# Kernel optimization log

Measured on AMD Instinct MI355X. Metric: run time of the kernel, lower is better.

The kernel has to match this reference:

```python
import jax, jax.numpy as jnp
import numpy as np

N = 50000      # nodes
E = 300000     # edges
F_IN = 128     # num_features
H = 256        # hidden_dim
C = 32         # num_classes


def gcn_conv(x, src, dst, W, b, num_nodes):
    """PyG-style GCNConv: add self-loops, sym-normalize, X W, scatter-add, + bias."""
    loop = jnp.arange(num_nodes, dtype=src.dtype)
    src2 = jnp.concatenate([src, loop])          # [E+N]
    dst2 = jnp.concatenate([dst, loop])          # [E+N]
    # degree of target nodes (with self-loops, unit edge weights)
    deg = jax.ops.segment_sum(jnp.ones_like(dst2, dtype=x.dtype), dst2,
                              num_segments=num_nodes)
    dinv = jnp.where(deg > 0, jax.lax.rsqrt(deg), 0.0)
    norm = dinv[src2] * dinv[dst2]               # [E+N]
    h = x @ W                                    # [N, out]  dense GEMM first (PyG order)
    msg = h[src2] * norm[:, None]                # gather + scale  [E+N, out]
    out = jax.ops.segment_sum(msg, dst2, num_segments=num_nodes)  # scatter-add
    return out + b


def setup_inputs() -> dict:
    key = jax.random.key(0)
    ks = jax.random.split(key, 8)
    x = jax.random.normal(ks[0], (N, F_IN), dtype=jnp.float32)
    edge_index = jax.random.randint(ks[1], (2, E), 0, N, dtype=jnp.int64)
    W1 = jax.random.normal(ks[2], (F_IN, H), dtype=jnp.float32) / np.float32(np.sqrt(F_IN))
    b1 = jnp.zeros((H,), jnp.float32)
    W2 = jax.random.normal(ks[3], (H, H), dtype=jnp.float32) / np.float32(np.sqrt(H))
    b2 = jnp.zeros((H,), jnp.float32)
    Wc = jax.random.normal(ks[4], (H, C), dtype=jnp.float32) / np.float32(np.sqrt(H))
    bc = jnp.zeros((C,), jnp.float32)
    return {"x": x, "edge_index": edge_index, "W1": W1, "b1": b1,
            "W2": W2, "b2": b2, "Wc": Wc, "bc": bc}


def reference(x, edge_index, W1, b1, W2, b2, Wc, bc):
    src, dst = edge_index[0], edge_index[1]
    h = gcn_conv(x, src, dst, W1, b1, N)
    h = jax.nn.relu(h)                 # dropout is identity in eval mode
    h = gcn_conv(h, src, dst, W2, b2, N)
    h = jax.nn.relu(h)
    return h @ Wc + bc                 # [N, C]
```

## Files before the change

### kernel.cpp

```cpp
#include <hip/hip_runtime.h>
#include <math.h>

using short8 = __attribute__((ext_vector_type(8))) short;
using f32x4 = __attribute__((ext_vector_type(4))) float;

#define CAP 48

__device__ inline short f2bf(float f) {
    unsigned u = __builtin_bit_cast(unsigned, f);
    unsigned r = (u + 0x7fffu + ((u >> 16) & 1u)) >> 16;
    return (short)r;
}
__device__ inline float bf2f(short s) {
    unsigned u = ((unsigned)(unsigned short)s) << 16;
    return __builtin_bit_cast(float, u);
}

typedef const void __attribute__((address_space(1))) gvoid_t;
typedef void __attribute__((address_space(3))) svoid_t;
__device__ inline void gload16(const short* g, short* l) {
    __builtin_amdgcn_global_load_lds((gvoid_t*)g, (svoid_t*)l, 16, 0, 0);
}


__global__ void prep_kernel(const float* __restrict__ x, const float* __restrict__ W1,
                            const float* __restrict__ W2, const float* __restrict__ Wc,
                            const int* __restrict__ src, const int* __restrict__ dst,
                            short* __restrict__ xb, short* __restrict__ Wt1,
                            short* __restrict__ Wt2, short* __restrict__ Wtc,
                            int* __restrict__ deg, int* __restrict__ eslot,
                            int n, int e) {
    int idx = blockIdx.x * blockDim.x + threadIdx.x;
    const int nx8 = n * 16;
    if (idx < nx8) {
        const float4* p = (const float4*)x + (size_t)idx * 2;
        float4 v0 = p[0], v1 = p[1];
        short8 o;
        o[0] = f2bf(v0.x); o[1] = f2bf(v0.y); o[2] = f2bf(v0.z); o[3] = f2bf(v0.w);
        o[4] = f2bf(v1.x); o[5] = f2bf(v1.y); o[6] = f2bf(v1.z); o[7] = f2bf(v1.w);
        ((short8*)xb)[idx] = o;
        return;
    }
    idx -= nx8;
    if (idx < 128 * 256) {
        int k = idx >> 8, c = idx & 255;
        Wt1[c * 128 + k] = f2bf(W1[idx]);
        return;
    }
    idx -= 128 * 256;
    if (idx < 256 * 256) {
        int k = idx >> 8, c = idx & 255;
        Wt2[c * 256 + k] = f2bf(W2[idx]);
        return;
    }
    idx -= 256 * 256;
    if (idx < 256 * 32) {
        int k = idx >> 5, c = idx & 31;
        Wtc[c * 256 + k] = f2bf(Wc[idx]);
        return;
    }
    idx -= 256 * 32;
    if (idx < e) {
        int d = dst[idx], s = src[idx];
        int pos = atomicAdd(&deg[d], 1);
        if (pos < CAP) eslot[(size_t)d * CAP + pos] = s;
    }
}


template<bool RELU_BF16OUT>
__global__ __launch_bounds__(256) void mfma_gemm128_kernel(
    const short* __restrict__ A, const short* __restrict__ Wt,
    const float* __restrict__ bias, void* __restrict__ Cout,
    int M, int K, int NC)
{
    __shared__ short As[128 * 32];
    __shared__ short Bs[128 * 32];

    const int tid = threadIdx.x;
    const int wave = tid >> 6, lane = tid & 63;
    const int m0 = blockIdx.y * 128, n0 = blockIdx.x * 128;
    const int wm = (wave >> 1) * 64, wn = (wave & 1) * 64;

    const int lr0 = tid >> 2;
    const int lr1 = 64 + lr0;
    const int cdst = tid & 3;
    const int cg0 = cdst ^ ((lr0 >> 1) & 3);
    const int cg1 = cdst ^ ((lr1 >> 1) & 3);
    int ga0 = m0 + lr0; if (ga0 >= M) ga0 = M - 1;
    int ga1 = m0 + lr1; if (ga1 >= M) ga1 = M - 1;
    int gb0 = n0 + lr0; if (gb0 >= NC) gb0 = NC - 1;
    int gb1 = n0 + lr1; if (gb1 >= NC) gb1 = NC - 1;
    const short* pa0 = A + (size_t)ga0 * K + cg0 * 8;
    const short* pa1 = A + (size_t)ga1 * K + cg1 * 8;
    const short* pb0 = Wt + (size_t)gb0 * K + cg0 * 8;
    const short* pb1 = Wt + (size_t)gb1 * K + cg1 * 8;

    short* lA0 = &As[(wave * 16) * 32];
    short* lA1 = &As[(64 + wave * 16) * 32];
    short* lB0 = &Bs[(wave * 16) * 32];
    short* lB1 = &Bs[(64 + wave * 16) * 32];

    f32x4 acc[4][4] = {};
    const int fr = lane & 15;
    const int cfrag = lane >> 4;
    const int swzr = (fr >> 1) & 3;

    for (int k0 = 0; k0 < K; k0 += 32) {
        gload16(pa0 + k0, lA0);
        gload16(pa1 + k0, lA1);
        gload16(pb0 + k0, lB0);
        gload16(pb1 + k0, lB1);
        __syncthreads();

        short8 af[4], bfv[4];
        #pragma unroll
        for (int mt = 0; mt < 4; ++mt) {
            int rr = wm + mt * 16 + fr;
            af[mt] = *(const short8*)&As[rr * 32 + ((cfrag ^ swzr) << 3)];
        }
        #pragma unroll
        for (int nt = 0; nt < 4; ++nt) {
            int rr = wn + nt * 16 + fr;
            bfv[nt] = *(const short8*)&Bs[rr * 32 + ((cfrag ^ swzr) << 3)];
        }

        #pragma unroll
        for (int mt = 0; mt < 4; ++mt)
            #pragma unroll
            for (int nt = 0; nt < 4; ++nt)
                acc[mt][nt] = __builtin_amdgcn_mfma_f32_16x16x32_bf16(
                    af[mt], bfv[nt], acc[mt][nt], 0, 0, 0);

        __syncthreads();
    }

    #pragma unroll
    for (int mt = 0; mt < 4; ++mt) {
        #pragma unroll
        for (int nt = 0; nt < 4; ++nt) {
            #pragma unroll
            for (int r = 0; r < 4; ++r) {
                int grow = m0 + wm + mt * 16 + (lane >> 4) * 4 + r;
                int gcol = n0 + wn + nt * 16 + (lane & 15);
                if (grow < M && gcol < NC) {
                    float v = acc[mt][nt][r] + bias[gcol];
                    if (RELU_BF16OUT)
                        ((short*)Cout)[(size_t)grow * NC + gcol] = f2bf(fmaxf(v, 0.f));
                    else
                        ((float*)Cout)[(size_t)grow * NC + gcol] = v;
                }
            }
        }
    }
}


__global__ __launch_bounds__(512, 4) void layer2_fused_kernel(
    const short* __restrict__ hA,
    const int* __restrict__ deg, const int* __restrict__ eslot,
    const short* __restrict__ Wt2,
    const float* __restrict__ b2,
    const short* __restrict__ Wtc,
    const float* __restrict__ bc,
    float* __restrict__ out,
    int M)
{
    const int K = 256;
    __shared__ short smem[128 * 256 + 256 * 32];
    short* hT = smem;
    short* Bs = smem + 128 * 256;

    const int tid = threadIdx.x;
    const int wave = tid >> 6, lane = tid & 63;
    const int m0 = blockIdx.x * 128;

    const int srow = tid >> 2;
    const int cdst = tid & 3;
    const int lrB0 = srow, lrB1 = 128 + srow;
    const int cg0 = cdst ^ ((lrB0 >> 1) & 3);
    const int cg1 = cdst ^ ((lrB1 >> 1) & 3);
    const short* pb0 = Wt2 + (size_t)lrB0 * K + cg0 * 8;
    const short* pb1 = Wt2 + (size_t)lrB1 * K + cg1 * 8;
    short* lB0 = &Bs[(wave * 16) * 32];
    short* lB1 = &Bs[(128 + wave * 16) * 32];

    gload16(pb0, lB0);
    gload16(pb1, lB1);

    {
        const int grp = tid >> 5;
        const int gl  = tid & 31;
        const int f   = gl * 8;
        const int wslot = (gl >> 2) * 32;
        for (int r0 = 0; r0 < 128; r0 += 16) {
            int r = r0 + grp;
            int node = m0 + r; if (node >= M) node = M - 1;
            int dg = deg[node];
            if (dg > CAP) dg = CAP;
            float di = rsqrtf((float)dg + 1.0f);
            float w = di * di;
            short8 hv = *(const short8*)(hA + (size_t)node * 256 + f);
            float a[8];
            #pragma unroll
            for (int j = 0; j < 8; ++j) a[j] = bf2f(hv[j]) * w;

            const int* bucket = eslot + (size_t)node * CAP;
            for (int e = 0; e < dg; e += 4) {
                int4 s4 = *(const int4*)(bucket + e);
                int i0 = s4.x;
                int i1 = (e + 1 < dg) ? s4.y : 0;
                int i2 = (e + 2 < dg) ? s4.z : 0;
                int i3 = (e + 3 < dg) ? s4.w : 0;
                int d0 = deg[i0], d1 = deg[i1], d2 = deg[i2], d3 = deg[i3];
                short8 v0 = *(const short8*)(hA + (size_t)i0 * 256 + f);
                short8 v1 = *(const short8*)(hA + (size_t)i1 * 256 + f);
                short8 v2 = *(const short8*)(hA + (size_t)i2 * 256 + f);
                short8 v3 = *(const short8*)(hA + (size_t)i3 * 256 + f);
                float w0 = rsqrtf((float)d0 + 1.0f) * di;
                float w1 = (e + 1 < dg) ? rsqrtf((float)d1 + 1.0f) * di : 0.f;
                float w2 = (e + 2 < dg) ? rsqrtf((float)d2 + 1.0f) * di : 0.f;
                float w3 = (e + 3 < dg) ? rsqrtf((float)d3 + 1.0f) * di : 0.f;
                #pragma unroll
                for (int j = 0; j < 8; ++j) {
                    a[j] = fmaf(bf2f(v0[j]), w0, a[j]);
                    a[j] = fmaf(bf2f(v1[j]), w1, a[j]);
                    a[j] = fmaf(bf2f(v2[j]), w2, a[j]);
                    a[j] = fmaf(bf2f(v3[j]), w3, a[j]);
                }
            }
            short8 o;
            #pragma unroll
            for (int j = 0; j < 8; ++j) o[j] = f2bf(a[j]);
            int slot = (gl & 3) ^ ((r >> 1) & 3);
            *(short8*)&hT[r * 256 + wslot + slot * 8] = o;
        }
    }

    const int wm = (wave >> 2) * 64;
    const int wn = (wave & 3) * 64;
    const int fr = lane & 15;
    const int cfrag = lane >> 4;
    const int swzr = (fr >> 1) & 3;

    f32x4 acc[4][4] = {};
    for (int k0 = 0; k0 < K; k0 += 32) {
        __syncthreads();

        short8 af[4], bfv[4];
        #pragma unroll
        for (int mt = 0; mt < 4; ++mt) {
            int rr = wm + mt * 16 + fr;
            af[mt] = *(const short8*)&hT[rr * 256 + k0 + ((cfrag ^ swzr) << 3)];
        }
        #pragma unroll
        for (int nt = 0; nt < 4; ++nt) {
            int rr = wn + nt * 16 + fr;
            bfv[nt] = *(const short8*)&Bs[rr * 32 + ((cfrag ^ swzr) << 3)];
        }

        __syncthreads();
        if (k0 + 32 < K) {
            gload16(pb0 + k0 + 32, lB0);
            gload16(pb1 + k0 + 32, lB1);
        }

        #pragma unroll
        for (int mt = 0; mt < 4; ++mt)
            #pragma unroll
            for (int nt = 0; nt < 4; ++nt)
                acc[mt][nt] = __builtin_amdgcn_mfma_f32_16x16x32_bf16(
                    af[mt], bfv[nt], acc[mt][nt], 0, 0, 0);
    }

    #pragma unroll
    for (int mt = 0; mt < 4; ++mt) {
        #pragma unroll
        for (int nt = 0; nt < 4; ++nt) {
            #pragma unroll
            for (int r = 0; r < 4; ++r) {
                int lrow = wm + mt * 16 + (lane >> 4) * 4 + r;
                int gcol = wn + nt * 16 + fr;
                float v = acc[mt][nt][r] + b2[gcol];
                int slot = ((gcol >> 3) & 3) ^ ((lrow >> 1) & 3);
                hT[lrow * 256 + (gcol >> 5) * 32 + slot * 8 + (gcol & 7)] =
                    f2bf(fmaxf(v, 0.f));
            }
        }
    }
    __syncthreads();

    f32x4 c2[2] = {};
    for (int k0 = 0; k0 < K; k0 += 32) {
        int row = wave * 16 + fr;
        short8 a8 = *(const short8*)&hT[row * 256 + k0 + ((cfrag ^ swzr) << 3)];
        #pragma unroll
        for (int nt = 0; nt < 2; ++nt) {
            short8 b8 = *(const short8*)(Wtc + (size_t)(nt * 16 + fr) * K +
                                         (cfrag << 3) + k0);
            c2[nt] = __builtin_amdgcn_mfma_f32_16x16x32_bf16(a8, b8, c2[nt], 0, 0, 0);
        }
    }
    #pragma unroll
    for (int nt = 0; nt < 2; ++nt) {
        #pragma unroll
        for (int r = 0; r < 4; ++r) {
            int grow = m0 + wave * 16 + (lane >> 4) * 4 + r;
            int gcol = nt * 16 + fr;
            if (grow < M)
                out[(size_t)grow * 32 + gcol] = c2[nt][r] + bc[gcol];
        }
    }
}


template<int LPN>
__global__ __launch_bounds__(256) void gather_kernel(
    const short* __restrict__ h, const int* __restrict__ deg,
    const int* __restrict__ eslot, short* __restrict__ out, int n)
{
    const int F = LPN * 8;
    int node = (blockIdx.x * 256 + threadIdx.x) / LPN;
    if (node >= n) return;
    int lane = threadIdx.x % LPN;
    int f = lane * 8;

    int dg = deg[node];
    if (dg > CAP) dg = CAP;
    float di = rsqrtf((float)dg + 1.0f);
    float w = di * di;

    const size_t rb = (size_t)node * F + f;
    short8 hv = *(const short8*)(h + rb);
    float a[8];
    #pragma unroll
    for (int j = 0; j < 8; ++j) a[j] = bf2f(hv[j]) * w;

    const int* bucket = eslot + (size_t)node * CAP;
    for (int e = 0; e < dg; e += 4) {
        int4 s4 = *(const int4*)(bucket + e);
        int i0 = s4.x;
        int i1 = (e + 1 < dg) ? s4.y : 0;
        int i2 = (e + 2 < dg) ? s4.z : 0;
        int i3 = (e + 3 < dg) ? s4.w : 0;
        int d0 = deg[i0], d1 = deg[i1], d2 = deg[i2], d3 = deg[i3];
        short8 v0 = *(const short8*)(h + (size_t)i0 * F + f);
        short8 v1 = *(const short8*)(h + (size_t)i1 * F + f);
        short8 v2 = *(const short8*)(h + (size_t)i2 * F + f);
        short8 v3 = *(const short8*)(h + (size_t)i3 * F + f);
        float w0 = rsqrtf((float)d0 + 1.0f) * di;
        float w1 = (e + 1 < dg) ? rsqrtf((float)d1 + 1.0f) * di : 0.f;
        float w2 = (e + 2 < dg) ? rsqrtf((float)d2 + 1.0f) * di : 0.f;
        float w3 = (e + 3 < dg) ? rsqrtf((float)d3 + 1.0f) * di : 0.f;
        #pragma unroll
        for (int j = 0; j < 8; ++j) {
            a[j] = fmaf(bf2f(v0[j]), w0, a[j]);
            a[j] = fmaf(bf2f(v1[j]), w1, a[j]);
            a[j] = fmaf(bf2f(v2[j]), w2, a[j]);
            a[j] = fmaf(bf2f(v3[j]), w3, a[j]);
        }
    }
    short8 o;
    #pragma unroll
    for (int j = 0; j < 8; ++j) o[j] = f2bf(a[j]);
    *(short8*)(out + rb) = o;
}


extern "C" void kernel_launch(void* const* d_in, const int* in_sizes, int n_in,
                              void* d_out, int out_size, void* d_ws, size_t ws_size,
                              hipStream_t stream) {
    const float* x  = (const float*)d_in[0];
    const int*   ei = (const int*)d_in[1];
    const float* W1 = (const float*)d_in[2];
    const float* b1 = (const float*)d_in[3];
    const float* W2 = (const float*)d_in[4];
    const float* b2 = (const float*)d_in[5];
    const float* Wc = (const float*)d_in[6];
    const float* bc = (const float*)d_in[7];
    float* out = (float*)d_out;

    const int E = in_sizes[1] / 2;
    const int N = in_sizes[0] / 128;
    const int F_IN = 128, H = 256;
    const int* src = ei;
    const int* dst = ei + E;

    short* xb   = (short*)d_ws;
    short* aggX = xb + (size_t)N * 128;
    short* hA   = aggX + (size_t)N * 128;
    short* Wt1  = hA + (size_t)N * 256;
    short* Wt2  = Wt1 + 256 * 128;
    short* Wtc  = Wt2 + 256 * 256;
    int*   deg  = (int*)(Wtc + 32 * 256);
    int*   eslot= deg + N;

    const int TB = 256;

    hipMemsetAsync(deg, 0, (size_t)N * sizeof(int), stream);

    const int prep_total = N * 16 + 128 * 256 + 256 * 256 + 256 * 32 + E;
    prep_kernel<<<(prep_total + TB - 1) / TB, TB, 0, stream>>>(
        x, W1, W2, Wc, src, dst, xb, Wt1, Wt2, Wtc, deg, eslot, N, E);

    const int gy = (N + 127) / 128;

    gather_kernel<16><<<((size_t)N * 16 + TB - 1) / TB, TB, 0, stream>>>(
        xb, deg, eslot, aggX, N);
    mfma_gemm128_kernel<true><<<dim3(H / 128, gy), 256, 0, stream>>>(aggX, Wt1, b1, hA, N, F_IN, H);

    layer2_fused_kernel<<<gy, 512, 0, stream>>>(
        hA, deg, eslot, Wt2, b2, Wtc, bc, out, N);
}
```

Measured before the change: 195.1 us.

## Read W2 fragments straight from global and pad the LDS tile instead of swizzling

The fused layer-2 kernel no longer stages W2 tiles into LDS with async global-to-LDS loads and per-k-step barriers. B fragments are now read directly from global memory (cache-resident W2), and the aggregated tile uses a padded row stride (264) instead of an XOR swizzle. This removes two barriers per k-step and frees LDS. In exchange, global load latency sits in the MFMA loop, and the 16-byte padding may leave some LDS bank conflicts.

```diff
diff --git a/kernel.cpp b/kernel.cpp
--- a/kernel.cpp
+++ b/kernel.cpp
@@ -167,32 +167,17 @@
     int M)
 {
     const int K = 256;
-    __shared__ short smem[128 * 256 + 256 * 32];
-    short* hT = smem;
-    short* Bs = smem + 128 * 256;
+    const int TP = 264;
+    __shared__ short hT[128 * 264];
 
     const int tid = threadIdx.x;
     const int wave = tid >> 6, lane = tid & 63;
     const int m0 = blockIdx.x * 128;
-
-    const int srow = tid >> 2;
-    const int cdst = tid & 3;
-    const int lrB0 = srow, lrB1 = 128 + srow;
-    const int cg0 = cdst ^ ((lrB0 >> 1) & 3);
-    const int cg1 = cdst ^ ((lrB1 >> 1) & 3);
-    const short* pb0 = Wt2 + (size_t)lrB0 * K + cg0 * 8;
-    const short* pb1 = Wt2 + (size_t)lrB1 * K + cg1 * 8;
-    short* lB0 = &Bs[(wave * 16) * 32];
-    short* lB1 = &Bs[(128 + wave * 16) * 32];
-
-    gload16(pb0, lB0);
-    gload16(pb1, lB1);
 
     {
         const int grp = tid >> 5;
         const int gl  = tid & 31;
         const int f   = gl * 8;
-        const int wslot = (gl >> 2) * 32;
         for (int r0 = 0; r0 < 128; r0 += 16) {
             int r = r0 + grp;
             int node = m0 + r; if (node >= M) node = M - 1;
@@ -232,38 +217,25 @@
             short8 o;
             #pragma unroll
             for (int j = 0; j < 8; ++j) o[j] = f2bf(a[j]);
-            int slot = (gl & 3) ^ ((r >> 1) & 3);
-            *(short8*)&hT[r * 256 + wslot + slot * 8] = o;
-        }
-    }
+            *(short8*)&hT[r * TP + f] = o;
+        }
+    }
+    __syncthreads();
 
     const int wm = (wave >> 2) * 64;
     const int wn = (wave & 3) * 64;
     const int fr = lane & 15;
-    const int cfrag = lane >> 4;
-    const int swzr = (fr >> 1) & 3;
+    const int fk = (lane >> 4) * 8;
 
     f32x4 acc[4][4] = {};
     for (int k0 = 0; k0 < K; k0 += 32) {
-        __syncthreads();
-
         short8 af[4], bfv[4];
         #pragma unroll
-        for (int mt = 0; mt < 4; ++mt) {
-            int rr = wm + mt * 16 + fr;
-            af[mt] = *(const short8*)&hT[rr * 256 + k0 + ((cfrag ^ swzr) << 3)];
-        }
-        #pragma unroll
-        for (int nt = 0; nt < 4; ++nt) {
-            int rr = wn + nt * 16 + fr;
-            bfv[nt] = *(const short8*)&Bs[rr * 32 + ((cfrag ^ swzr) << 3)];
-        }
-
-        __syncthreads();
-        if (k0 + 32 < K) {
-            gload16(pb0 + k0 + 32, lB0);
-            gload16(pb1 + k0 + 32, lB1);
-        }
+        for (int mt = 0; mt < 4; ++mt)
+            af[mt] = *(const short8*)&hT[(wm + mt * 16 + fr) * TP + k0 + fk];
+        #pragma unroll
+        for (int nt = 0; nt < 4; ++nt)
+            bfv[nt] = *(const short8*)(Wt2 + (size_t)(wn + nt * 16 + fr) * K + k0 + fk);
 
         #pragma unroll
         for (int mt = 0; mt < 4; ++mt)
@@ -272,6 +244,7 @@
                 acc[mt][nt] = __builtin_amdgcn_mfma_f32_16x16x32_bf16(
                     af[mt], bfv[nt], acc[mt][nt], 0, 0, 0);
     }
+    __syncthreads();
 
     #pragma unroll
     for (int mt = 0; mt < 4; ++mt) {
@@ -282,9 +255,7 @@
                 int lrow = wm + mt * 16 + (lane >> 4) * 4 + r;
                 int gcol = wn + nt * 16 + fr;
                 float v = acc[mt][nt][r] + b2[gcol];
-                int slot = ((gcol >> 3) & 3) ^ ((lrow >> 1) & 3);
-                hT[lrow * 256 + (gcol >> 5) * 32 + slot * 8 + (gcol & 7)] =
-                    f2bf(fmaxf(v, 0.f));
+                hT[lrow * TP + gcol] = f2bf(fmaxf(v, 0.f));
             }
         }
     }
@@ -292,12 +263,10 @@
 
     f32x4 c2[2] = {};
     for (int k0 = 0; k0 < K; k0 += 32) {
-        int row = wave * 16 + fr;
-        short8 a8 = *(const short8*)&hT[row * 256 + k0 + ((cfrag ^ swzr) << 3)];
+        short8 a8 = *(const short8*)&hT[(wave * 16 + fr) * TP + k0 + fk];
         #pragma unroll
         for (int nt = 0; nt < 2; ++nt) {
-            short8 b8 = *(const short8*)(Wtc + (size_t)(nt * 16 + fr) * K +
-                                         (cfrag << 3) + k0);
+            short8 b8 = *(const short8*)(Wtc + (size_t)(nt * 16 + fr) * K + k0 + fk);
             c2[nt] = __builtin_amdgcn_mfma_f32_16x16x32_bf16(a8, b8, c2[nt], 0, 0, 0);
         }
     }
```

New measurement: 200.5 us. 2.8% more time.

## Fuse layer-1 neighbor aggregation into the layer-1 MFMA GEMM kernel

Applied to the files above, without the earlier changes.

Replaces the separate gather kernel and the layer-1 GEMM with one kernel. Each 512-thread block aggregates 128 node rows of normalized neighbor features into an LDS tile (XOR-swizzled), then multiplies that tile by W1 with bf16 MFMA while prefetching the next W1 slab. This removes the aggX round trip through global memory and one launch. In exchange, each block computes all 256 output columns, uses more LDS, and runs the irregular gather at lower parallelism than the standalone gather kernel.

```diff
diff --git a/kernel.cpp b/kernel.cpp
--- a/kernel.cpp
+++ b/kernel.cpp
@@ -68,71 +68,116 @@
 }
 
 
-template<bool RELU_BF16OUT>
-__global__ __launch_bounds__(256) void mfma_gemm128_kernel(
-    const short* __restrict__ A, const short* __restrict__ Wt,
-    const float* __restrict__ bias, void* __restrict__ Cout,
-    int M, int K, int NC)
+__global__ __launch_bounds__(512, 4) void layer1_fused_kernel(
+    const short* __restrict__ xb,
+    const int* __restrict__ deg, const int* __restrict__ eslot,
+    const short* __restrict__ Wt1,
+    const float* __restrict__ b1,
+    short* __restrict__ hA,
+    int M)
 {
-    __shared__ short As[128 * 32];
-    __shared__ short Bs[128 * 32];
+    const int K = 128;
+    __shared__ short hT[128 * 128];
+    __shared__ short Bs[256 * 32];
 
     const int tid = threadIdx.x;
     const int wave = tid >> 6, lane = tid & 63;
-    const int m0 = blockIdx.y * 128, n0 = blockIdx.x * 128;
-    const int wm = (wave >> 1) * 64, wn = (wave & 1) * 64;
-
-    const int lr0 = tid >> 2;
-    const int lr1 = 64 + lr0;
+    const int m0 = blockIdx.x * 128;
+
+    const int srow = tid >> 2;
     const int cdst = tid & 3;
-    const int cg0 = cdst ^ ((lr0 >> 1) & 3);
-    const int cg1 = cdst ^ ((lr1 >> 1) & 3);
-    int ga0 = m0 + lr0; if (ga0 >= M) ga0 = M - 1;
-    int ga1 = m0 + lr1; if (ga1 >= M) ga1 = M - 1;
-    int gb0 = n0 + lr0; if (gb0 >= NC) gb0 = NC - 1;
-    int gb1 = n0 + lr1; if (gb1 >= NC) gb1 = NC - 1;
-    const short* pa0 = A + (size_t)ga0 * K + cg0 * 8;
-    const short* pa1 = A + (size_t)ga1 * K + cg1 * 8;
-    const short* pb0 = Wt + (size_t)gb0 * K + cg0 * 8;
-    const short* pb1 = Wt + (size_t)gb1 * K + cg1 * 8;
-
-    short* lA0 = &As[(wave * 16) * 32];
-    short* lA1 = &As[(64 + wave * 16) * 32];
+    const int lrB0 = srow, lrB1 = 128 + srow;
+    const int cg0 = cdst ^ ((lrB0 >> 1) & 3);
+    const int cg1 = cdst ^ ((lrB1 >> 1) & 3);
+    const short* pb0 = Wt1 + (size_t)lrB0 * K + cg0 * 8;
+    const short* pb1 = Wt1 + (size_t)lrB1 * K + cg1 * 8;
     short* lB0 = &Bs[(wave * 16) * 32];
-    short* lB1 = &Bs[(64 + wave * 16) * 32];
-
-    f32x4 acc[4][4] = {};
+    short* lB1 = &Bs[(128 + wave * 16) * 32];
+
+    gload16(pb0, lB0);
+    gload16(pb1, lB1);
+
+    {
+        const int grp = tid >> 4;
+        const int gl  = tid & 15;
+        const int f   = gl * 8;
+        for (int r0 = 0; r0 < 128; r0 += 32) {
+            int r = r0 + grp;
+            int node = m0 + r; if (node >= M) node = M - 1;
+            int dg = deg[node];
+            if (dg > CAP) dg = CAP;
+            float di = rsqrtf((float)dg + 1.0f);
+            float w = di * di;
+            short8 hv = *(const short8*)(xb + (size_t)node * 128 + f);
+            float a[8];
+            #pragma unroll
+            for (int j = 0; j < 8; ++j) a[j] = bf2f(hv[j]) * w;
+
+            const int* bucket = eslot + (size_t)node * CAP;
+            for (int e = 0; e < dg; e += 4) {
+                int4 s4 = *(const int4*)(bucket + e);
+                int i0 = s4.x;
+                int i1 = (e + 1 < dg) ? s4.y : 0;
+                int i2 = (e + 2 < dg) ? s4.z : 0;
+                int i3 = (e + 3 < dg) ? s4.w : 0;
+                int d0 = deg[i0], d1 = deg[i1], d2 = deg[i2], d3 = deg[i3];
+                short8 v0 = *(const short8*)(xb + (size_t)i0 * 128 + f);
+                short8 v1 = *(const short8*)(xb + (size_t)i1 * 128 + f);
+                short8 v2 = *(const short8*)(xb + (size_t)i2 * 128 + f);
+                short8 v3 = *(const short8*)(xb + (size_t)i3 * 128 + f);
+                float w0 = rsqrtf((float)d0 + 1.0f) * di;
+                float w1 = (e + 1 < dg) ? rsqrtf((float)d1 + 1.0f) * di : 0.f;
+                float w2 = (e + 2 < dg) ? rsqrtf((float)d2 + 1.0f) * di : 0.f;
+                float w3 = (e + 3 < dg) ? rsqrtf((float)d3 + 1.0f) * di : 0.f;
+                #pragma unroll
+                for (int j = 0; j < 8; ++j) {
+                    a[j] = fmaf(bf2f(v0[j]), w0, a[j]);
+                    a[j] = fmaf(bf2f(v1[j]), w1, a[j]);
+                    a[j] = fmaf(bf2f(v2[j]), w2, a[j]);
+                    a[j] = fmaf(bf2f(v3[j]), w3, a[j]);
+                }
+            }
+            short8 o;
+            #pragma unroll
+            for (int j = 0; j < 8; ++j) o[j] = f2bf(a[j]);
+            *(short8*)&hT[r * 128 + ((gl ^ (r & 7)) << 3)] = o;
+        }
+    }
+
+    const int wm = (wave >> 2) * 64;
+    const int wn = (wave & 3) * 64;
     const int fr = lane & 15;
     const int cfrag = lane >> 4;
+    const int rk = fr & 7;
     const int swzr = (fr >> 1) & 3;
 
+    f32x4 acc[4][4] = {};
     for (int k0 = 0; k0 < K; k0 += 32) {
-        gload16(pa0 + k0, lA0);
-        gload16(pa1 + k0, lA1);
-        gload16(pb0 + k0, lB0);
-        gload16(pb1 + k0, lB1);
         __syncthreads();
 
+        const int cswz = (((k0 >> 3) + cfrag) ^ rk) << 3;
         short8 af[4], bfv[4];
         #pragma unroll
-        for (int mt = 0; mt < 4; ++mt) {
-            int rr = wm + mt * 16 + fr;
-            af[mt] = *(const short8*)&As[rr * 32 + ((cfrag ^ swzr) << 3)];
-        }
+        for (int mt = 0; mt < 4; ++mt)
+            af[mt] = *(const short8*)&hT[(wm + mt * 16 + fr) * 128 + cswz];
         #pragma unroll
         for (int nt = 0; nt < 4; ++nt) {
             int rr = wn + nt * 16 + fr;
             bfv[nt] = *(const short8*)&Bs[rr * 32 + ((cfrag ^ swzr) << 3)];
         }
 
+        __syncthreads();
+        if (k0 + 32 < K) {
+            gload16(pb0 + k0 + 32, lB0);
+            gload16(pb1 + k0 + 32, lB1);
+        }
+
         #pragma unroll
         for (int mt = 0; mt < 4; ++mt)
             #pragma unroll
             for (int nt = 0; nt < 4; ++nt)
                 acc[mt][nt] = __builtin_amdgcn_mfma_f32_16x16x32_bf16(
                     af[mt], bfv[nt], acc[mt][nt], 0, 0, 0);
-
-        __syncthreads();
     }
 
     #pragma unroll
@@ -142,13 +187,10 @@
             #pragma unroll
             for (int r = 0; r < 4; ++r) {
                 int grow = m0 + wm + mt * 16 + (lane >> 4) * 4 + r;
-                int gcol = n0 + wn + nt * 16 + (lane & 15);
-                if (grow < M && gcol < NC) {
-                    float v = acc[mt][nt][r] + bias[gcol];
-                    if (RELU_BF16OUT)
-                        ((short*)Cout)[(size_t)grow * NC + gcol] = f2bf(fmaxf(v, 0.f));
-                    else
-                        ((float*)Cout)[(size_t)grow * NC + gcol] = v;
+                int gcol = wn + nt * 16 + fr;
+                if (grow < M) {
+                    float v = acc[mt][nt][r] + b1[gcol];
+                    hA[(size_t)grow * 256 + gcol] = f2bf(fmaxf(v, 0.f));
                 }
             }
         }
@@ -314,59 +356,6 @@
 }
 
 
-template<int LPN>
-__global__ __launch_bounds__(256) void gather_kernel(
-    const short* __restrict__ h, const int* __restrict__ deg,
-    const int* __restrict__ eslot, short* __restrict__ out, int n)
-{
-    const int F = LPN * 8;
-    int node = (blockIdx.x * 256 + threadIdx.x) / LPN;
-    if (node >= n) return;
-    int lane = threadIdx.x % LPN;
-    int f = lane * 8;
-
-    int dg = deg[node];
-    if (dg > CAP) dg = CAP;
-    float di = rsqrtf((float)dg + 1.0f);
-    float w = di * di;
-
-    const size_t rb = (size_t)node * F + f;
-    short8 hv = *(const short8*)(h + rb);
-    float a[8];
-    #pragma unroll
-    for (int j = 0; j < 8; ++j) a[j] = bf2f(hv[j]) * w;
-
-    const int* bucket = eslot + (size_t)node * CAP;
-    for (int e = 0; e < dg; e += 4) {
-        int4 s4 = *(const int4*)(bucket + e);
-        int i0 = s4.x;
-        int i1 = (e + 1 < dg) ? s4.y : 0;
-        int i2 = (e + 2 < dg) ? s4.z : 0;
-        int i3 = (e + 3 < dg) ? s4.w : 0;
-        int d0 = deg[i0], d1 = deg[i1], d2 = deg[i2], d3 = deg[i3];
-        short8 v0 = *(const short8*)(h + (size_t)i0 * F + f);
-        short8 v1 = *(const short8*)(h + (size_t)i1 * F + f);
-        short8 v2 = *(const short8*)(h + (size_t)i2 * F + f);
-        short8 v3 = *(const short8*)(h + (size_t)i3 * F + f);
-        float w0 = rsqrtf((float)d0 + 1.0f) * di;
-        float w1 = (e + 1 < dg) ? rsqrtf((float)d1 + 1.0f) * di : 0.f;
-        float w2 = (e + 2 < dg) ? rsqrtf((float)d2 + 1.0f) * di : 0.f;
-        float w3 = (e + 3 < dg) ? rsqrtf((float)d3 + 1.0f) * di : 0.f;
-        #pragma unroll
-        for (int j = 0; j < 8; ++j) {
-            a[j] = fmaf(bf2f(v0[j]), w0, a[j]);
-            a[j] = fmaf(bf2f(v1[j]), w1, a[j]);
-            a[j] = fmaf(bf2f(v2[j]), w2, a[j]);
-            a[j] = fmaf(bf2f(v3[j]), w3, a[j]);
-        }
-    }
-    short8 o;
-    #pragma unroll
-    for (int j = 0; j < 8; ++j) o[j] = f2bf(a[j]);
-    *(short8*)(out + rb) = o;
-}
-
-
 extern "C" void kernel_launch(void* const* d_in, const int* in_sizes, int n_in,
                               void* d_out, int out_size, void* d_ws, size_t ws_size,
                               hipStream_t stream) {
@@ -382,13 +371,11 @@
 
     const int E = in_sizes[1] / 2;
     const int N = in_sizes[0] / 128;
-    const int F_IN = 128, H = 256;
     const int* src = ei;
     const int* dst = ei + E;
 
     short* xb   = (short*)d_ws;
-    short* aggX = xb + (size_t)N * 128;
-    short* hA   = aggX + (size_t)N * 128;
+    short* hA   = xb + (size_t)N * 128;
     short* Wt1  = hA + (size_t)N * 256;
     short* Wt2  = Wt1 + 256 * 128;
     short* Wtc  = Wt2 + 256 * 256;
@@ -405,9 +392,8 @@
 
     const int gy = (N + 127) / 128;
 
-    gather_kernel<16><<<((size_t)N * 16 + TB - 1) / TB, TB, 0, stream>>>(
-        xb, deg, eslot, aggX, N);
-    mfma_gemm128_kernel<true><<<dim3(H / 128, gy), 256, 0, stream>>>(aggX, Wt1, b1, hA, N, F_IN, H);
+    layer1_fused_kernel<<<gy, 512, 0, stream>>>(
+        xb, deg, eslot, Wt1, b1, hA, N);
 
     layer2_fused_kernel<<<gy, 512, 0, stream>>>(
         hA, deg, eslot, Wt2, b2, Wtc, bc, out, N);
```

Result: faster. 182.2 us (-6.6%).
